# Kernel tuning notes

Measured on AMD Instinct MI355X. Metric: run time of the kernel, lower is better.

The kernel has to match this reference:

```python
import jax, jax.numpy as jnp
import numpy as np
from jax import lax

# Model dimensions (from init_kwargs)
I_SIZE, H_SIZE, O_SIZE = 256, 512, 256
N_NEURONS = I_SIZE + H_SIZE + O_SIZE   # 1024
N_ACTIVE = H_SIZE + O_SIZE             # 768 neurons in range(I_SIZE, N_NEURONS)
N_DIMS = 64
D_FEAT = 128


def _sphere(k, shape):
    # geoopt.Sphere().projx == L2 normalization of rows
    v = jax.random.normal(k, shape, dtype=jnp.float32)
    return v / jnp.linalg.norm(v, axis=-1, keepdims=True)


def setup_inputs() -> dict:
    key = jax.random.key(0)
    k0, k1, k2, k3, k4 = jax.random.split(key, 5)
    return {
        "x": jax.random.normal(k0, (I_SIZE, D_FEAT), dtype=jnp.float32),          # x[i] for input index i
        "pos_head": _sphere(k1, (N_NEURONS, N_DIMS)),
        "pos_tail": _sphere(k2, (N_NEURONS, N_DIMS)),
        "W": jax.random.normal(k3, (N_ACTIVE, D_FEAT, D_FEAT), dtype=jnp.float32) / np.float32(np.sqrt(D_FEAT)),
        "a": jax.random.normal(k4, (N_ACTIVE, N_NEURONS), dtype=jnp.float32),
    }


def reference(x, pos_head, pos_tail, W, a):
    # add_to_state: data_pos = tail positions of input indices 0..I_SIZE-1
    data_pos = pos_tail[:I_SIZE]                      # [i, n_dims]
    # _score: data_pos @ heads.T
    scores = data_pos @ pos_head.T                    # [i, n_neurons]
    # tau is identity per the source (self.tau = [lambda x: x ...]), so scores unchanged.
    # _aggregate: einsum('ij,kl->lj', data, scores) -> [n_neurons, d_feat]
    agg = jnp.einsum('ij,kl->lj', x, scores)
    # Per-neuron sequential transform loop over active indices range(I_SIZE, N_NEURONS):
    #   data = transforms[idx](data[order]);  transform_i(v) = tanh(outer(a_i, v @ W_i))
    orders = jnp.arange(N_ACTIVE)

    def step(carry, inp):
        Wt, at, t = inp
        v = carry[t]                                  # gather row `order` [d_feat]
        new = jnp.tanh(jnp.outer(at, v @ Wt))         # [n_neurons, d_feat]
        return new, new

    _, outs = lax.scan(step, agg, (W, a, orders))     # [n_active, n_neurons, d_feat]
    # First O_SIZE active indices lie in the output range [I_SIZE, I_SIZE+O_SIZE):
    # those iterations populate `out`; later (hidden) iterations only update state.
    return outs[:O_SIZE]                              # [o_size, n_neurons, d_feat]
```

## Files before the change

kernel.cpp:

```cpp
#include <hip/hip_runtime.h>
#include <math.h>

#define D_FEAT   128
#define O_SIZE   256
#define N_NEUR   1024
#define STEPS_PER_WG 4
#define N_CHAIN_WG   (O_SIZE / STEPS_PER_WG)
#define N_WRITER_WG  192
#define N_BLOCKS     (N_CHAIN_WG + N_WRITER_WG)
#define N_ITEMS      (O_SIZE * 8)

typedef unsigned long long ull;
typedef float floatx4 __attribute__((ext_vector_type(4)));

__device__ ull      g_chan[N_CHAIN_WG][D_FEAT];
__device__ ull      g_uchan[O_SIZE][D_FEAT];
__device__ unsigned g_uflag[O_SIZE];
__device__ unsigned g_gen  = 1u;
__device__ int      g_done = 0;

__device__ __forceinline__ float tanh_fast(float x) {
    x = fminf(fmaxf(x, -20.f), 20.f);
    float e = __expf(2.f * x);
    return (e - 1.f) * __builtin_amdgcn_rcpf(e + 1.f);
}

__global__ __launch_bounds__(1024) void fused_kernel(
    const float* __restrict__ x,
    const float* __restrict__ pos_head,
    const float* __restrict__ pos_tail,
    const float* __restrict__ W,
    const float* __restrict__ a,
    float* __restrict__ out)
{
    const int bid = blockIdx.x;
    const int tid = threadIdx.x;
    const unsigned gen = g_gen;

    if (bid < N_CHAIN_WG) {
        __shared__ float v_lds[D_FEAT];
        __shared__ float psum[8][D_FEAT];
        __shared__ float ptps[8][64];
        __shared__ float red[64];

        const int g  = ((bid & 7) << 3) | (bid >> 3);
        const int s  = tid >> 7;
        const int j  = tid & 127;
        const int t0 = g * STEPS_PER_WG;

        float w[STEPS_PER_WG][16];
        #pragma unroll
        for (int k = 0; k < STEPS_PER_WG; ++k) {
            #pragma unroll
            for (int m = 0; m < 16; ++m)
                w[k][m] = W[((size_t)(t0 + k) * D_FEAT + (s * 16 + m)) * D_FEAT + j];
        }
        float ascal[STEPS_PER_WG];
        #pragma unroll
        for (int k = 0; k < STEPS_PER_WG; ++k)
            ascal[k] = a[(t0 + k) * N_NEUR + (t0 + k) + 1];

        if (g == 0) {
            {
                float acc = 0.f;
                #pragma unroll 8
                for (int ii = 0; ii < 32; ++ii)
                    acc += x[(s * 32 + ii) * D_FEAT + j];
                psum[s][j] = acc;
            }
            if (tid < 512) {
                const int kb = tid >> 6, d = tid & 63;
                float acc = 0.f;
                #pragma unroll 8
                for (int kk = 0; kk < 32; ++kk)
                    acc += pos_tail[(kb * 32 + kk) * 64 + d];
                ptps[kb][d] = acc;
            }
            __syncthreads();
            if (tid < 64) {
                float ptd = 0.f;
                #pragma unroll
                for (int kb = 0; kb < 8; ++kb) ptd += ptps[kb][tid];
                red[tid] = ptd * pos_head[tid];
            }
            __syncthreads();
            if (tid < 128) {
                float sx = 0.f;
                #pragma unroll
                for (int s8 = 0; s8 < 8; ++s8) sx += psum[s8][tid];
                float ss0 = 0.f;
                #pragma unroll
                for (int d = 0; d < 64; ++d) ss0 += red[d];
                v_lds[tid] = ss0 * sx;
            }
        }

        float dummy = 0.f;
        #pragma unroll
        for (int k = 0; k < STEPS_PER_WG; ++k) {
            #pragma unroll
            for (int m = 0; m < 16; ++m) {
                asm volatile("" : "+v"(w[k][m]));
                dummy += w[k][m];
            }
            asm volatile("" : "+v"(ascal[k]));
        }
        asm volatile("" :: "v"(dummy));

        if (g > 0 && tid < 128) {
            const unsigned want = (gen << 8) | (unsigned)g;
            ull pk;
            for (;;) {
                pk = __hip_atomic_load(&g_chan[g][j], __ATOMIC_RELAXED,
                                       __HIP_MEMORY_SCOPE_AGENT);
                if ((unsigned)(pk >> 32) == want) break;
                __builtin_amdgcn_s_sleep(1);
            }
            v_lds[j] = __uint_as_float((unsigned)pk);
        }
        __syncthreads();

        float ureg[STEPS_PER_WG];
        #pragma unroll
        for (int k = 0; k < STEPS_PER_WG; ++k) {
            float acc = 0.f;
            #pragma unroll
            for (int m = 0; m < 16; ++m)
                acc += v_lds[s * 16 + m] * w[k][m];
            psum[s][j] = acc;
            __syncthreads();

            if (tid < 128) {
                float u = 0.f;
                #pragma unroll
                for (int ss = 0; ss < 8; ++ss) u += psum[ss][j];
                ureg[k] = u;
                const float vn = tanh_fast(ascal[k] * u);
                if (k < STEPS_PER_WG - 1) {
                    v_lds[j] = vn;
                } else if (g + 1 < N_CHAIN_WG) {
                    const ull pk = (((ull)((gen << 8) | (unsigned)(g + 1))) << 32) |
                                   (ull)__float_as_uint(vn);
                    __hip_atomic_store(&g_chan[g + 1][j], pk, __ATOMIC_RELAXED,
                                       __HIP_MEMORY_SCOPE_AGENT);
                }
            }
            __syncthreads();
        }

        if (tid < 128) {
            #pragma unroll
            for (int k = 0; k < STEPS_PER_WG; ++k) {
                const int t = t0 + k;
                const ull upk = (((ull)((gen << 8) | (unsigned)t)) << 32) |
                                (ull)__float_as_uint(ureg[k]);
                __hip_atomic_store(&g_uchan[t][j], upk, __ATOMIC_RELAXED,
                                   __HIP_MEMORY_SCOPE_AGENT);
            }
        }
        __syncthreads();
        if (tid < STEPS_PER_WG) {
            const int t = t0 + tid;
            __hip_atomic_store(&g_uflag[t], (gen << 8) | (unsigned)t,
                               __ATOMIC_RELAXED, __HIP_MEMORY_SCOPE_AGENT);
        }
    } else {
        const int wid = bid - N_CHAIN_WG;
        const int j4  = tid & 31;
        for (int i = wid; i < N_ITEMS; i += N_WRITER_WG) {
            const int t = i >> 3;
            const int c = i & 7;
            const unsigned want = (gen << 8) | (unsigned)t;
            if (tid == 0) {
                while (__hip_atomic_load(&g_uflag[t], __ATOMIC_RELAXED,
                                         __HIP_MEMORY_SCOPE_AGENT) != want)
                    __builtin_amdgcn_s_sleep(8);
            }
            __syncthreads();

            const ull e0 = __hip_atomic_load(&g_uchan[t][4 * j4 + 0], __ATOMIC_RELAXED, __HIP_MEMORY_SCOPE_AGENT);
            const ull e1 = __hip_atomic_load(&g_uchan[t][4 * j4 + 1], __ATOMIC_RELAXED, __HIP_MEMORY_SCOPE_AGENT);
            const ull e2 = __hip_atomic_load(&g_uchan[t][4 * j4 + 2], __ATOMIC_RELAXED, __HIP_MEMORY_SCOPE_AGENT);
            const ull e3 = __hip_atomic_load(&g_uchan[t][4 * j4 + 3], __ATOMIC_RELAXED, __HIP_MEMORY_SCOPE_AGENT);
            const float u0 = __uint_as_float((unsigned)e0);
            const float u1 = __uint_as_float((unsigned)e1);
            const float u2 = __uint_as_float((unsigned)e2);
            const float u3 = __uint_as_float((unsigned)e3);

            const int lbase = (c << 7) + (tid >> 5);
            #pragma unroll
            for (int p = 0; p < 4; ++p) {
                const int row = (t << 10) + lbase + (p << 5);
                const float sc = a[row];
                floatx4 r;
                r.x = tanh_fast(sc * u0);
                r.y = tanh_fast(sc * u1);
                r.z = tanh_fast(sc * u2);
                r.w = tanh_fast(sc * u3);
                __builtin_nontemporal_store(r, (floatx4*)out + (((size_t)row) << 5) + j4);
            }
        }
    }

    __syncthreads();
    if (tid == 0) {
        const int old = atomicAdd(&g_done, 1);
        if (old == N_BLOCKS - 1) {
            __hip_atomic_store(&g_done, 0, __ATOMIC_RELAXED, __HIP_MEMORY_SCOPE_AGENT);
            __hip_atomic_store(&g_gen, gen + 1u, __ATOMIC_RELAXED, __HIP_MEMORY_SCOPE_AGENT);
        }
    }
}

extern "C" void kernel_launch(void* const* d_in, const int* in_sizes, int n_in,
                              void* d_out, int out_size, void* d_ws, size_t ws_size,
                              hipStream_t stream)
{
    const float* x        = (const float*)d_in[0];
    const float* pos_head = (const float*)d_in[1];
    const float* pos_tail = (const float*)d_in[2];
    const float* W        = (const float*)d_in[3];
    const float* a        = (const float*)d_in[4];
    float*       out      = (float*)d_out;

    hipLaunchKernelGGL(fused_kernel, dim3(N_BLOCKS), dim3(1024), 0, stream,
                       x, pos_head, pos_tail, W, a, out);
}
```

Before: 291.9 us.

## Reduce chain matvec partials with wave shuffles and double-buffered LDS vector

Remaps each chain workgroup's threads so that the 8 partial sums for one output column sit in the same wavefront. They are combined with xor-shuffles instead of being written to an LDS psum array and read back after a barrier. This removes one __syncthreads per serial step. The vector is now double-buffered in LDS and read as float4, so the next step's writes do not race with the current step's reads. The W loads change access pattern (8 contiguous columns per lane group), which may make the one-time preload less coalesced.

```diff
diff --git a/kernel.cpp b/kernel.cpp
--- a/kernel.cpp
+++ b/kernel.cpp
@@ -38,22 +38,24 @@
     const unsigned gen = g_gen;
 
     if (bid < N_CHAIN_WG) {
-        __shared__ float v_lds[D_FEAT];
-        __shared__ float psum[8][D_FEAT];
+        __shared__ __align__(16) float v_lds[2][D_FEAT];
+        __shared__ float psum0[8][D_FEAT];
         __shared__ float ptps[8][64];
         __shared__ float red[64];
 
-        const int g  = ((bid & 7) << 3) | (bid >> 3);
-        const int s  = tid >> 7;
-        const int j  = tid & 127;
-        const int t0 = g * STEPS_PER_WG;
+        const int g   = ((bid & 7) << 3) | (bid >> 3);
+        const int wv  = tid >> 6;
+        const int l   = tid & 63;
+        const int grp = l >> 3;
+        const int j   = (wv << 3) | (l & 7);
+        const int t0  = g * STEPS_PER_WG;
 
         float w[STEPS_PER_WG][16];
         #pragma unroll
         for (int k = 0; k < STEPS_PER_WG; ++k) {
             #pragma unroll
-            for (int m = 0; m < 16; ++m)
-                w[k][m] = W[((size_t)(t0 + k) * D_FEAT + (s * 16 + m)) * D_FEAT + j];
+            for (int kk = 0; kk < 16; ++kk)
+                w[k][kk] = W[((size_t)(t0 + k) * D_FEAT + (grp * 16 + kk)) * D_FEAT + j];
         }
         float ascal[STEPS_PER_WG];
         #pragma unroll
@@ -62,11 +64,12 @@
 
         if (g == 0) {
             {
+                const int s = tid >> 7, jx = tid & 127;
                 float acc = 0.f;
                 #pragma unroll 8
                 for (int ii = 0; ii < 32; ++ii)
-                    acc += x[(s * 32 + ii) * D_FEAT + j];
-                psum[s][j] = acc;
+                    acc += x[(s * 32 + ii) * D_FEAT + jx];
+                psum0[s][jx] = acc;
             }
             if (tid < 512) {
                 const int kb = tid >> 6, d = tid & 63;
@@ -87,58 +90,61 @@
             if (tid < 128) {
                 float sx = 0.f;
                 #pragma unroll
-                for (int s8 = 0; s8 < 8; ++s8) sx += psum[s8][tid];
+                for (int s8 = 0; s8 < 8; ++s8) sx += psum0[s8][tid];
                 float ss0 = 0.f;
                 #pragma unroll
                 for (int d = 0; d < 64; ++d) ss0 += red[d];
-                v_lds[tid] = ss0 * sx;
-            }
-        }
-
-        float dummy = 0.f;
-        #pragma unroll
-        for (int k = 0; k < STEPS_PER_WG; ++k) {
-            #pragma unroll
-            for (int m = 0; m < 16; ++m) {
-                asm volatile("" : "+v"(w[k][m]));
-                dummy += w[k][m];
-            }
-            asm volatile("" : "+v"(ascal[k]));
-        }
-        asm volatile("" :: "v"(dummy));
-
-        if (g > 0 && tid < 128) {
-            const unsigned want = (gen << 8) | (unsigned)g;
-            ull pk;
-            for (;;) {
-                pk = __hip_atomic_load(&g_chan[g][j], __ATOMIC_RELAXED,
-                                       __HIP_MEMORY_SCOPE_AGENT);
-                if ((unsigned)(pk >> 32) == want) break;
-                __builtin_amdgcn_s_sleep(1);
-            }
-            v_lds[j] = __uint_as_float((unsigned)pk);
+                v_lds[0][tid] = ss0 * sx;
+            }
+        } else {
+            float dummy = 0.f;
+            #pragma unroll
+            for (int k = 0; k < STEPS_PER_WG; ++k) {
+                #pragma unroll
+                for (int kk = 0; kk < 16; ++kk) {
+                    asm volatile("" : "+v"(w[k][kk]));
+                    dummy += w[k][kk];
+                }
+                asm volatile("" : "+v"(ascal[k]));
+            }
+            asm volatile("" :: "v"(dummy));
+
+            if (tid < 128) {
+                const unsigned want = (gen << 8) | (unsigned)g;
+                ull pk;
+                for (;;) {
+                    pk = __hip_atomic_load(&g_chan[g][tid], __ATOMIC_RELAXED,
+                                           __HIP_MEMORY_SCOPE_AGENT);
+                    if ((unsigned)(pk >> 32) == want) break;
+                    __builtin_amdgcn_s_sleep(1);
+                }
+                v_lds[0][tid] = __uint_as_float((unsigned)pk);
+            }
         }
         __syncthreads();
 
         float ureg[STEPS_PER_WG];
         #pragma unroll
         for (int k = 0; k < STEPS_PER_WG; ++k) {
-            float acc = 0.f;
-            #pragma unroll
-            for (int m = 0; m < 16; ++m)
-                acc += v_lds[s * 16 + m] * w[k][m];
-            psum[s][j] = acc;
-            __syncthreads();
-
-            if (tid < 128) {
-                float u = 0.f;
-                #pragma unroll
-                for (int ss = 0; ss < 8; ++ss) u += psum[ss][j];
-                ureg[k] = u;
-                const float vn = tanh_fast(ascal[k] * u);
-                if (k < STEPS_PER_WG - 1) {
-                    v_lds[j] = vn;
-                } else if (g + 1 < N_CHAIN_WG) {
+            const floatx4* v4 = (const floatx4*)v_lds[k & 1];
+            const floatx4 b0 = v4[grp * 4 + 0];
+            const floatx4 b1 = v4[grp * 4 + 1];
+            const floatx4 b2 = v4[grp * 4 + 2];
+            const floatx4 b3 = v4[grp * 4 + 3];
+            float acc;
+            acc  = b0.x * w[k][ 0] + b0.y * w[k][ 1] + b0.z * w[k][ 2] + b0.w * w[k][ 3];
+            acc += b1.x * w[k][ 4] + b1.y * w[k][ 5] + b1.z * w[k][ 6] + b1.w * w[k][ 7];
+            acc += b2.x * w[k][ 8] + b2.y * w[k][ 9] + b2.z * w[k][10] + b2.w * w[k][11];
+            acc += b3.x * w[k][12] + b3.y * w[k][13] + b3.z * w[k][14] + b3.w * w[k][15];
+            acc += __shfl_xor(acc, 8);
+            acc += __shfl_xor(acc, 16);
+            acc += __shfl_xor(acc, 32);
+            ureg[k] = acc;
+            const float vn = tanh_fast(ascal[k] * acc);
+            if (k < STEPS_PER_WG - 1) {
+                if (grp == 0) v_lds[(k + 1) & 1][j] = vn;
+            } else if (g + 1 < N_CHAIN_WG) {
+                if (grp == 0) {
                     const ull pk = (((ull)((gen << 8) | (unsigned)(g + 1))) << 32) |
                                    (ull)__float_as_uint(vn);
                     __hip_atomic_store(&g_chan[g + 1][j], pk, __ATOMIC_RELAXED,
@@ -148,7 +154,7 @@
             __syncthreads();
         }
 
-        if (tid < 128) {
+        if (grp == 0) {
             #pragma unroll
             for (int k = 0; k < STEPS_PER_WG; ++k) {
                 const int t = t0 + k;
```

Result: slower. 299.7 us (+2.7%).

## Throttle chain polling with a progress counter and vectorize the per-step matvec

Applied to the files above, without the earlier changes.

Adds a global progress counter so each chain workgroup only begins busy-polling its channel once the workgroup two positions upstream has started. This is meant to cut memory-system contention from many spinning pollers on the critical serial chain. It also reads v_lds with 16-byte vector loads and splits the dot product and partial-sum reductions into shorter dependency trees to reduce per-step latency. The extra counter adds an atomic store per workgroup, and a delayed start could add latency if the throttle wakes late.

```diff
diff --git a/kernel.cpp b/kernel.cpp
--- a/kernel.cpp
+++ b/kernel.cpp
@@ -16,6 +16,7 @@
 __device__ ull      g_chan[N_CHAIN_WG][D_FEAT];
 __device__ ull      g_uchan[O_SIZE][D_FEAT];
 __device__ unsigned g_uflag[O_SIZE];
+__device__ unsigned g_prog = 0;
 __device__ unsigned g_gen  = 1u;
 __device__ int      g_done = 0;
 
@@ -38,7 +39,7 @@
     const unsigned gen = g_gen;
 
     if (bid < N_CHAIN_WG) {
-        __shared__ float v_lds[D_FEAT];
+        __shared__ __align__(16) float v_lds[D_FEAT];
         __shared__ float psum[8][D_FEAT];
         __shared__ float ptps[8][64];
         __shared__ float red[64];
@@ -93,47 +94,69 @@
                 for (int d = 0; d < 64; ++d) ss0 += red[d];
                 v_lds[tid] = ss0 * sx;
             }
-        }
-
-        float dummy = 0.f;
-        #pragma unroll
-        for (int k = 0; k < STEPS_PER_WG; ++k) {
-            #pragma unroll
-            for (int m = 0; m < 16; ++m) {
-                asm volatile("" : "+v"(w[k][m]));
-                dummy += w[k][m];
-            }
-            asm volatile("" : "+v"(ascal[k]));
-        }
-        asm volatile("" :: "v"(dummy));
-
-        if (g > 0 && tid < 128) {
-            const unsigned want = (gen << 8) | (unsigned)g;
-            ull pk;
-            for (;;) {
-                pk = __hip_atomic_load(&g_chan[g][j], __ATOMIC_RELAXED,
-                                       __HIP_MEMORY_SCOPE_AGENT);
-                if ((unsigned)(pk >> 32) == want) break;
-                __builtin_amdgcn_s_sleep(1);
-            }
-            v_lds[j] = __uint_as_float((unsigned)pk);
+        } else {
+            float dummy = 0.f;
+            #pragma unroll
+            for (int k = 0; k < STEPS_PER_WG; ++k) {
+                #pragma unroll
+                for (int m = 0; m < 16; ++m) {
+                    asm volatile("" : "+v"(w[k][m]));
+                    dummy += w[k][m];
+                }
+                asm volatile("" : "+v"(ascal[k]));
+            }
+            asm volatile("" :: "v"(dummy));
+
+            if (g > 2 && tid == 0) {
+                const unsigned wantp = (unsigned)(g - 2);
+                for (;;) {
+                    const unsigned pv = __hip_atomic_load(&g_prog, __ATOMIC_RELAXED,
+                                                          __HIP_MEMORY_SCOPE_AGENT);
+                    if ((pv >> 8) == gen && (pv & 0xFFu) >= wantp) break;
+                    __builtin_amdgcn_s_sleep(16);
+                }
+            }
+            __syncthreads();
+
+            if (tid < 128) {
+                const unsigned want = (gen << 8) | (unsigned)g;
+                ull pk;
+                for (;;) {
+                    pk = __hip_atomic_load(&g_chan[g][tid], __ATOMIC_RELAXED,
+                                           __HIP_MEMORY_SCOPE_AGENT);
+                    if ((unsigned)(pk >> 32) == want) break;
+                    __builtin_amdgcn_s_sleep(1);
+                }
+                v_lds[tid] = __uint_as_float((unsigned)pk);
+            }
         }
         __syncthreads();
+
+        if (tid == 0)
+            __hip_atomic_store(&g_prog, (gen << 8) | (unsigned)g,
+                               __ATOMIC_RELAXED, __HIP_MEMORY_SCOPE_AGENT);
 
         float ureg[STEPS_PER_WG];
         #pragma unroll
         for (int k = 0; k < STEPS_PER_WG; ++k) {
-            float acc = 0.f;
-            #pragma unroll
-            for (int m = 0; m < 16; ++m)
-                acc += v_lds[s * 16 + m] * w[k][m];
-            psum[s][j] = acc;
+            const floatx4* v4 = (const floatx4*)&v_lds[s * 16];
+            const floatx4 b0 = v4[0];
+            const floatx4 b1 = v4[1];
+            const floatx4 b2 = v4[2];
+            const floatx4 b3 = v4[3];
+            float a0 = b0.x * w[k][ 0] + b0.y * w[k][ 1] + b0.z * w[k][ 2] + b0.w * w[k][ 3];
+            float a1 = b1.x * w[k][ 4] + b1.y * w[k][ 5] + b1.z * w[k][ 6] + b1.w * w[k][ 7];
+            float a2 = b2.x * w[k][ 8] + b2.y * w[k][ 9] + b2.z * w[k][10] + b2.w * w[k][11];
+            float a3 = b3.x * w[k][12] + b3.y * w[k][13] + b3.z * w[k][14] + b3.w * w[k][15];
+            psum[s][j] = (a0 + a1) + (a2 + a3);
             __syncthreads();
 
             if (tid < 128) {
-                float u = 0.f;
-                #pragma unroll
-                for (int ss = 0; ss < 8; ++ss) u += psum[ss][j];
+                const float p0 = psum[0][j] + psum[1][j];
+                const float p1 = psum[2][j] + psum[3][j];
+                const float p2 = psum[4][j] + psum[5][j];
+                const float p3 = psum[6][j] + psum[7][j];
+                const float u  = (p0 + p1) + (p2 + p3);
                 ureg[k] = u;
                 const float vn = tanh_fast(ascal[k] * u);
                 if (k < STEPS_PER_WG - 1) {
```

After: 359.8 us. 23.3% more time.
